# Performance work log

Measured on AMD Instinct MI355X. Metric: run time of the kernel, lower is better.

Reference implementation:

```python
import jax, jax.numpy as jnp
import numpy as np

GROUPS = 32
EPS = 1e-5

def setup_inputs() -> dict:
    key = jax.random.key(0)
    ks = jax.random.split(key, 10)
    B, H, W, C = 2, 64, 64, 512
    s = 1.0 / np.sqrt(C)
    return {
        "x": jax.random.normal(ks[0], (B, H, W, C), dtype=jnp.float32),
        "gamma": jnp.ones((C,), jnp.float32),
        "beta": jnp.zeros((C,), jnp.float32),
        "wq": jax.random.normal(ks[1], (C, C), jnp.float32) * s,
        "bq": jnp.zeros((C,), jnp.float32),
        "wk": jax.random.normal(ks[2], (C, C), jnp.float32) * s,
        "bk": jnp.zeros((C,), jnp.float32),
        "wv": jax.random.normal(ks[3], (C, C), jnp.float32) * s,
        "bv": jnp.zeros((C,), jnp.float32),
        "wp": jax.random.normal(ks[4], (C, C), jnp.float32) * s,
        "bp": jnp.zeros((C,), jnp.float32),
    }

def _group_norm(x, gamma, beta):
    B, H, W, C = x.shape
    xg = x.reshape(B, H, W, GROUPS, C // GROUPS)
    mean = jnp.mean(xg, axis=(1, 2, 4), keepdims=True)
    var = jnp.var(xg, axis=(1, 2, 4), keepdims=True)
    xg = (xg - mean) * jax.lax.rsqrt(var + EPS)
    return xg.reshape(B, H, W, C) * gamma + beta

def reference(x, gamma, beta, wq, bq, wk, bk, wv, bv, wp, bp):
    B, H, W, C = x.shape
    h_ = _group_norm(x, gamma, beta)
    # 1x1 convs are per-pixel linear maps
    q = jnp.einsum("bhwc,cd->bhwd", h_, wq) + bq
    k = jnp.einsum("bhwc,cd->bhwd", h_, wk) + bk
    v = jnp.einsum("bhwc,cd->bhwd", h_, wv) + bv
    q = q.reshape(B, H * W, C)
    k = k.reshape(B, H * W, C)
    v = v.reshape(B, H * W, C)
    scale = C ** (-0.5)
    attn = jax.nn.softmax(jnp.einsum("bqc,bkc->bqk", q, k) * scale, axis=-1)
    out = jnp.einsum("bqk,bkc->bqc", attn, v).reshape(B, H, W, C)
    proj = jnp.einsum("bhwc,cd->bhwd", out, wp) + bp
    return x + proj
```

## Files before the change

### kernel.cpp

```cpp
#include <hip/hip_runtime.h>
#include <hip/hip_bf16.h>
#include <cstdint>
#include <cstddef>

typedef __bf16 bf16;
typedef bf16 bf16x8 __attribute__((ext_vector_type(8)));
typedef bf16 bf16x4 __attribute__((ext_vector_type(4)));
typedef float floatx4 __attribute__((ext_vector_type(4)));
typedef int intx8 __attribute__((ext_vector_type(8)));
typedef int intx4 __attribute__((ext_vector_type(4)));

#define DEVI __device__ __forceinline__

#define C_  512
#define HW_ 4096
#define B_  2
#define M_  8192
#define TK  64


DEVI floatx4 mfma16(bf16x8 a, bf16x8 b, floatx4 c) {
  return __builtin_amdgcn_mfma_f32_16x16x32_bf16(a, b, c, 0, 0, 0);
}

DEVI floatx4 mfma_fp8(intx8 a, intx8 b, floatx4 c) {
  return __builtin_amdgcn_mfma_scale_f32_16x16x128_f8f6f4(a, b, c, 0, 0,
                                                          0, 127, 0, 127);
}

DEVI void gload16(const void* g, void* lds) {
  using gp = const __attribute__((address_space(1))) unsigned int*;
  using lp = __attribute__((address_space(3))) unsigned int*;
  __builtin_amdgcn_global_load_lds(
      reinterpret_cast<gp>(reinterpret_cast<uintptr_t>(g)),
      reinterpret_cast<lp>((unsigned int)(uintptr_t)lds), 16, 0, 0);
}

DEVI uint32_t f32_to_fp8(float x) {
  return (uint32_t)__builtin_amdgcn_cvt_pk_fp8_f32(x, x, 0, false) & 0xffu;
}
DEVI int pack4_fp8(float a, float b, float c, float d) {
  int pk = __builtin_amdgcn_cvt_pk_fp8_f32(a, b, 0, false);
  return __builtin_amdgcn_cvt_pk_fp8_f32(c, d, pk, true);
}

__global__ __launch_bounds__(256) void gn_part(const float* __restrict__ x,
                                               float* __restrict__ pp,
                                               float* __restrict__ l) {
  int blk = blockIdx.x;
  int t = threadIdx.x;
  if (t < 16) l[blk * 16 + t] = 0.f;
  int batch = blk >> 8;
  int pix0 = (blk & 255) * 16;
  int c4 = (t & 127) << 2;
  int ph = t >> 7;
  const float* px = x + (size_t)batch * HW_ * C_ + (size_t)(pix0 + ph) * C_ + c4;
  float s1 = 0.f, s2 = 0.f;
#pragma unroll
  for (int i = 0; i < 8; i++) {
    float4 v = *reinterpret_cast<const float4*>(px + (size_t)i * 2 * C_);
    s1 += v.x + v.y + v.z + v.w;
    s2 += v.x * v.x + v.y * v.y + v.z * v.z + v.w * v.w;
  }
  __shared__ float l1[256], l2[256];
  l1[t] = s1; l2[t] = s2;
  __syncthreads();
  if (t < 32) {
    float a = 0.f, b2 = 0.f;
#pragma unroll
    for (int j = 0; j < 4; j++) {
      a  += l1[t * 4 + j] + l1[t * 4 + j + 128];
      b2 += l2[t * 4 + j] + l2[t * 4 + j + 128];
    }
    pp[blk * 32 + t] = a;
    pp[512 * 32 + blk * 32 + t] = b2;
  }
}

__global__ __launch_bounds__(256) void finish_wtrans(
    const float* __restrict__ pp, float* __restrict__ stats,
    const float* __restrict__ wq, const float* __restrict__ wk,
    const float* __restrict__ wv, const float* __restrict__ wp,
    uint8_t* __restrict__ w8, bf16* __restrict__ wtp) {
  int t = threadIdx.x;
  if (blockIdx.x < 64) {
    int bg = blockIdx.x;
    int b = bg >> 5, g = bg & 31;
    float s1 = pp[(b * 256 + t) * 32 + g];
    float s2 = pp[512 * 32 + (b * 256 + t) * 32 + g];
    for (int off = 32; off; off >>= 1) {
      s1 += __shfl_down(s1, off);
      s2 += __shfl_down(s2, off);
    }
    __shared__ float r1[4], r2[4];
    int wid = t >> 6;
    if ((t & 63) == 0) { r1[wid] = s1; r2[wid] = s2; }
    __syncthreads();
    if (t == 0) {
      s1 = r1[0] + r1[1] + r1[2] + r1[3];
      s2 = r2[0] + r2[1] + r2[2] + r2[3];
      float inv = 1.0f / (HW_ * 16);
      float mean = s1 * inv;
      float var  = s2 * inv - mean * mean;
      stats[bg]      = mean;
      stats[64 + bg] = rsqrtf(var + 1e-5f);
    }
    return;
  }
  int id = blockIdx.x - 64;
  int z = id >> 8;
  int k0 = ((id >> 4) & 15) * 32, n0 = (id & 15) * 32;
  const float* w = (z == 0) ? wq : (z == 1) ? wk : (z == 2) ? wv : wp;
  __shared__ float tt[32][33];
  int r = t >> 5, cc = t & 31;
  for (int i = 0; i < 4; i++) {
    int rr = r + i * 8;
    tt[rr][cc] = w[(size_t)(k0 + rr) * C_ + n0 + cc];
  }
  __syncthreads();
  if (z < 3) {
    uint8_t* dst = w8 + (size_t)z * C_ * C_;
    for (int i = 0; i < 4; i++) {
      int rr = r + i * 8;
      dst[(size_t)(n0 + rr) * C_ + k0 + cc] = (uint8_t)f32_to_fp8(tt[cc][rr]);
    }
  } else {
    for (int i = 0; i < 4; i++) {
      int rr = r + i * 8;
      wtp[(size_t)(n0 + rr) * C_ + k0 + cc] = (bf16)tt[cc][rr];
    }
  }
}

__global__ __launch_bounds__(256) void gn_apply(const float* __restrict__ x,
                                                const float* __restrict__ gamma,
                                                const float* __restrict__ beta,
                                                const float* __restrict__ stats,
                                                uint8_t* __restrict__ h8) {
  int idx = blockIdx.x * 256 + threadIdx.x;
  int m  = idx >> 7;
  int c4 = (idx & 127) << 2;
  int b = m >> 12;
  int g = c4 >> 4;
  float mean = stats[(b << 5) + g];
  float rs   = stats[64 + (b << 5) + g];
  const float4 xv = *reinterpret_cast<const float4*>(x + (size_t)m * C_ + c4);
  const float4 gv = *reinterpret_cast<const float4*>(gamma + c4);
  const float4 bv = *reinterpret_cast<const float4*>(beta + c4);
  int pk = pack4_fp8((xv.x - mean) * rs * gv.x + bv.x,
                     (xv.y - mean) * rs * gv.y + bv.y,
                     (xv.z - mean) * rs * gv.z + bv.z,
                     (xv.w - mean) * rs * gv.w + bv.w);
  *reinterpret_cast<int*>(h8 + (size_t)m * C_ + c4) = pk;
}

template <int BM, int BN, int MT, int NT>
DEVI void gemm_main(const bf16* __restrict__ A, int lda,
                    const bf16* __restrict__ Bt, int ldb,
                    int K, floatx4 (&acc)[MT][NT]) {
  constexpr int WCOLS = BN / (NT * 16);
  __shared__ __align__(16) bf16 As[BM * TK];
  __shared__ __align__(16) bf16 Bs[BN * TK];
  int tid = threadIdx.x;
  int w = tid >> 6, lane = tid & 63;
  int wrow = w / WCOLS, wcol = w % WCOLS;
  int col = lane & 15, quad = lane >> 4;
#pragma unroll
  for (int mt = 0; mt < MT; mt++)
#pragma unroll
    for (int nt = 0; nt < NT; nt++)
      acc[mt][nt] = floatx4{0.f, 0.f, 0.f, 0.f};
  for (int k0 = 0; k0 < K; k0 += TK) {
    __syncthreads();
#pragma unroll
    for (int i = 0; i < BM / 32; i++) {
      int id = tid + i * 256;
      int r = id >> 3, wd = id & 7;
      gload16(A + (size_t)r * lda + k0 + ((wd ^ (r & 7)) << 3), As + id * 8);
    }
#pragma unroll
    for (int i = 0; i < BN / 32; i++) {
      int id = tid + i * 256;
      int r = id >> 3, wd = id & 7;
      gload16(Bt + (size_t)r * ldb + k0 + ((wd ^ (r & 7)) << 3), Bs + id * 8);
    }
    __syncthreads();
#pragma unroll
    for (int kk = 0; kk < 2; kk++) {
      bf16x8 af[MT], bfr[NT];
#pragma unroll
      for (int mt = 0; mt < MT; mt++) {
        int rA = wrow * MT * 16 + mt * 16 + col;
        af[mt] = *reinterpret_cast<const bf16x8*>(
            As + rA * TK + (((kk * 4 + quad) ^ (rA & 7)) << 3));
      }
#pragma unroll
      for (int nt = 0; nt < NT; nt++) {
        int rB = wcol * NT * 16 + nt * 16 + col;
        bfr[nt] = *reinterpret_cast<const bf16x8*>(
            Bs + rB * TK + (((kk * 4 + quad) ^ (rB & 7)) << 3));
      }
#pragma unroll
      for (int mt = 0; mt < MT; mt++)
#pragma unroll
        for (int nt = 0; nt < NT; nt++)
          acc[mt][nt] = mfma16(af[mt], bfr[nt], acc[mt][nt]);
    }
  }
}

template <int BM, int BN, int MT, int NT>
DEVI void gemm_fp8(const uint8_t* __restrict__ A, int lda,
                   const uint8_t* __restrict__ Bt, int ldb,
                   int K, floatx4 (&acc)[MT][NT]) {
  constexpr int WCOLS = BN / (NT * 16);
  __shared__ __align__(16) uint8_t As[BM * 128];
  __shared__ __align__(16) uint8_t Bs[BN * 128];
  int tid = threadIdx.x;
  int w = tid >> 6, lane = tid & 63;
  int wrow = w / WCOLS, wcol = w % WCOLS;
  int col = lane & 15, quad = lane >> 4;
#pragma unroll
  for (int mt = 0; mt < MT; mt++)
#pragma unroll
    for (int nt = 0; nt < NT; nt++)
      acc[mt][nt] = floatx4{0.f, 0.f, 0.f, 0.f};
  for (int k0 = 0; k0 < K; k0 += 128) {
    __syncthreads();
#pragma unroll
    for (int i = 0; i < BM / 32; i++) {
      int id = tid + i * 256;
      int r = id >> 3, wd = id & 7;
      gload16(A + (size_t)r * lda + k0 + ((wd ^ (r & 7)) << 4), As + id * 16);
    }
#pragma unroll
    for (int i = 0; i < BN / 32; i++) {
      int id = tid + i * 256;
      int r = id >> 3, wd = id & 7;
      gload16(Bt + (size_t)r * ldb + k0 + ((wd ^ (r & 7)) << 4), Bs + id * 16);
    }
    __syncthreads();
    intx8 af[MT], bfr[NT];
#pragma unroll
    for (int mt = 0; mt < MT; mt++) {
      int rA = wrow * MT * 16 + mt * 16 + col;
      const uint8_t* rowp = As + (size_t)rA * 128;
      intx4 lo = *reinterpret_cast<const intx4*>(
          rowp + (((2 * quad) ^ (rA & 7)) << 4));
      intx4 hi = *reinterpret_cast<const intx4*>(
          rowp + (((2 * quad + 1) ^ (rA & 7)) << 4));
      af[mt] = __builtin_shufflevector(lo, hi, 0, 1, 2, 3, 4, 5, 6, 7);
    }
#pragma unroll
    for (int nt = 0; nt < NT; nt++) {
      int rB = wcol * NT * 16 + nt * 16 + col;
      const uint8_t* rowp = Bs + (size_t)rB * 128;
      intx4 lo = *reinterpret_cast<const intx4*>(
          rowp + (((2 * quad) ^ (rB & 7)) << 4));
      intx4 hi = *reinterpret_cast<const intx4*>(
          rowp + (((2 * quad + 1) ^ (rB & 7)) << 4));
      bfr[nt] = __builtin_shufflevector(lo, hi, 0, 1, 2, 3, 4, 5, 6, 7);
    }
#pragma unroll
    for (int mt = 0; mt < MT; mt++)
#pragma unroll
      for (int nt = 0; nt < NT; nt++)
        acc[mt][nt] = mfma_fp8(af[mt], bfr[nt], acc[mt][nt]);
  }
}

__global__ __launch_bounds__(256) void gemm_qkv(const uint8_t* __restrict__ h8,
                                                const uint8_t* __restrict__ w8,
                                                const float* __restrict__ bq,
                                                const float* __restrict__ bk,
                                                const float* __restrict__ bv,
                                                uint8_t* __restrict__ q8,
                                                uint8_t* __restrict__ k8,
                                                uint8_t* __restrict__ vt8) {
  int z = blockIdx.z;
  int m0 = blockIdx.x * 128, n0 = blockIdx.y * 128;
  floatx4 acc[4][4];
  gemm_fp8<128, 128, 4, 4>(h8 + (size_t)m0 * C_, C_,
                           w8 + (size_t)z * C_ * C_ + (size_t)n0 * C_, C_, C_, acc);
  int tid = threadIdx.x, w = tid >> 6, lane = tid & 63;
  int wrow = w >> 1, wcol = w & 1;
  int col = lane & 15, quad = lane >> 4;
  const float* bias = (z == 0) ? bq : (z == 1) ? bk : bv;
  if (z < 2) {
    uint8_t* out = (z == 0) ? q8 : k8;
#pragma unroll
    for (int mt = 0; mt < 4; mt++)
#pragma unroll
      for (int nt = 0; nt < 4; nt++) {
        int n = n0 + wcol * 64 + nt * 16 + col;
        float bb = bias[n];
#pragma unroll
        for (int r = 0; r < 4; r++) {
          int m = m0 + wrow * 64 + mt * 16 + quad * 4 + r;
          out[(size_t)m * C_ + n] = (uint8_t)f32_to_fp8(acc[mt][nt][r] + bb);
        }
      }
  } else {
#pragma unroll
    for (int mt = 0; mt < 4; mt++)
#pragma unroll
      for (int nt = 0; nt < 4; nt++) {
        int n = n0 + wcol * 64 + nt * 16 + col;
        float bb = bias[n];
        int mbase = m0 + wrow * 64 + mt * 16 + quad * 4;
        int b = mbase >> 12;
        int s = mbase & 4095;
        int pk = pack4_fp8(acc[mt][nt][0] + bb, acc[mt][nt][1] + bb,
                           acc[mt][nt][2] + bb, acc[mt][nt][3] + bb);
        *reinterpret_cast<int*>(vt8 + ((size_t)b * C_ + n) * HW_ + s) = pk;
      }
  }
}

__global__ __launch_bounds__(256) void gemm_qk(const uint8_t* __restrict__ q8,
                                               const uint8_t* __restrict__ k8,
                                               uint8_t* __restrict__ P8,
                                               float* __restrict__ l) {
  int b = blockIdx.z;
  int fid = blockIdx.y * 32 + blockIdx.x;
  int nid = (fid & 7) * 128 + (fid >> 3);
  int m0 = (nid & 31) * 128, n0 = (nid >> 5) * 128;
  floatx4 acc[4][4];
  gemm_fp8<128, 128, 4, 4>(q8 + ((size_t)b * HW_ + m0) * C_, C_,
                           k8 + ((size_t)b * HW_ + n0) * C_, C_, C_, acc);
  int tid = threadIdx.x, w = tid >> 6, lane = tid & 63;
  int wrow = w >> 1, wcol = w & 1;
  int col = lane & 15, quad = lane >> 4;
  const float sl2e = 0.044194173824159216f * 1.4426950408889634f;
  uint8_t* Pb = P8 + (size_t)b * HW_ * HW_;
  float* lb = l + (size_t)b * HW_;
#pragma unroll
  for (int mt = 0; mt < 4; mt++) {
    float rs[4] = {0.f, 0.f, 0.f, 0.f};
#pragma unroll
    for (int nt = 0; nt < 4; nt++) {
      int n = n0 + wcol * 64 + nt * 16 + col;
      float p0 = exp2f(acc[mt][nt][0] * sl2e);
      float p1 = exp2f(acc[mt][nt][1] * sl2e);
      float p2 = exp2f(acc[mt][nt][2] * sl2e);
      float p3 = exp2f(acc[mt][nt][3] * sl2e);
      int pk = pack4_fp8(p0, p1, p2, p3);
      size_t base = (size_t)(m0 + wrow * 64 + mt * 16 + quad * 4) * HW_ + n;
      Pb[base]           = (uint8_t)pk;
      Pb[base + HW_]     = (uint8_t)((unsigned)pk >> 8);
      Pb[base + 2 * HW_] = (uint8_t)((unsigned)pk >> 16);
      Pb[base + 3 * HW_] = (uint8_t)((unsigned)pk >> 24);
      rs[0] += p0; rs[1] += p1; rs[2] += p2; rs[3] += p3;
    }
#pragma unroll
    for (int off = 1; off < 16; off <<= 1)
#pragma unroll
      for (int r = 0; r < 4; r++)
        rs[r] += __shfl_xor(rs[r], off);
    if (col == 0)
#pragma unroll
      for (int r = 0; r < 4; r++)
        atomicAdd(&lb[m0 + wrow * 64 + mt * 16 + quad * 4 + r], rs[r]);
  }
}

__global__ __launch_bounds__(256) void gemm_pv(const uint8_t* __restrict__ P8,
                                               const uint8_t* __restrict__ vt8,
                                               const float* __restrict__ l,
                                               bf16* __restrict__ o) {
  int b = blockIdx.z;
  int m0 = blockIdx.x * 128, n0 = blockIdx.y * 64;
  floatx4 acc[2][4];
  gemm_fp8<128, 64, 2, 4>(P8 + (size_t)b * HW_ * HW_ + (size_t)m0 * HW_, HW_,
                          vt8 + ((size_t)b * C_ + n0) * HW_, HW_, HW_, acc);
  int tid = threadIdx.x, w = tid >> 6, lane = tid & 63;
  int col = lane & 15, quad = lane >> 4;
  const float* lb = l + (size_t)b * HW_;
  bf16* ob = o + (size_t)b * HW_ * C_;
#pragma unroll
  for (int mt = 0; mt < 2; mt++)
#pragma unroll
    for (int r = 0; r < 4; r++) {
      int m = m0 + w * 32 + mt * 16 + quad * 4 + r;
      float inv = 1.0f / lb[m];
#pragma unroll
      for (int nt = 0; nt < 4; nt++) {
        int n = n0 + nt * 16 + col;
        ob[(size_t)m * C_ + n] = (bf16)(acc[mt][nt][r] * inv);
      }
    }
}

__global__ __launch_bounds__(256) void gemm_proj(const bf16* __restrict__ o,
                                                 const bf16* __restrict__ wtp,
                                                 const float* __restrict__ bp,
                                                 const float* __restrict__ x,
                                                 float* __restrict__ out) {
  int m0 = blockIdx.x * 128, n0 = blockIdx.y * 128;
  floatx4 acc[4][4];
  gemm_main<128, 128, 4, 4>(o + (size_t)m0 * C_, C_, wtp + (size_t)n0 * C_, C_, C_, acc);
  int tid = threadIdx.x, w = tid >> 6, lane = tid & 63;
  int wrow = w >> 1, wcol = w & 1;
  int col = lane & 15, quad = lane >> 4;
#pragma unroll
  for (int mt = 0; mt < 4; mt++)
#pragma unroll
    for (int nt = 0; nt < 4; nt++) {
      int n = n0 + wcol * 64 + nt * 16 + col;
      float bb = bp[n];
#pragma unroll
      for (int r = 0; r < 4; r++) {
        int m = m0 + wrow * 64 + mt * 16 + quad * 4 + r;
        out[(size_t)m * C_ + n] = x[(size_t)m * C_ + n] + acc[mt][nt][r] + bb;
      }
    }
}

extern "C" void kernel_launch(void* const* d_in, const int* in_sizes, int n_in,
                              void* d_out, int out_size, void* d_ws, size_t ws_size,
                              hipStream_t stream) {
  const float* x     = (const float*)d_in[0];
  const float* gamma = (const float*)d_in[1];
  const float* beta  = (const float*)d_in[2];
  const float* wq    = (const float*)d_in[3];
  const float* bq    = (const float*)d_in[4];
  const float* wk    = (const float*)d_in[5];
  const float* bk    = (const float*)d_in[6];
  const float* wv    = (const float*)d_in[7];
  const float* bv    = (const float*)d_in[8];
  const float* wp    = (const float*)d_in[9];
  const float* bp    = (const float*)d_in[10];
  float* out = (float*)d_out;

  char* w8s = (char*)d_ws;
  float* stats = (float*)(w8s);
  float* l     = (float*)(w8s + 65536u);
  float* pp    = (float*)(w8s + 393216u);
  uint8_t* w8  = (uint8_t*)(w8s + (1u << 20));
  bf16* wtp    = (bf16*)(w8s + (2u << 20));
  uint8_t* h8  = (uint8_t*)(w8s + (4u << 20));
  bf16* o      = (bf16*)(w8s + (8u << 20));
  uint8_t* q8  = (uint8_t*)(w8s + (16u << 20));
  uint8_t* k8  = (uint8_t*)(w8s + (20u << 20));
  uint8_t* vt8 = (uint8_t*)(w8s + (24u << 20));
  uint8_t* P8  = (uint8_t*)(w8s + (28u << 20));

  gn_part<<<512, 256, 0, stream>>>(x, pp, l);
  finish_wtrans<<<1088, 256, 0, stream>>>(pp, stats, wq, wk, wv, wp, w8, wtp);
  gn_apply<<<4096, 256, 0, stream>>>(x, gamma, beta, stats, h8);
  gemm_qkv<<<dim3(M_ / 128, C_ / 128, 3), 256, 0, stream>>>(h8, w8, bq, bk, bv, q8, k8, vt8);
  gemm_qk<<<dim3(HW_ / 128, HW_ / 128, B_), 256, 0, stream>>>(q8, k8, P8, l);
  gemm_pv<<<dim3(HW_ / 128, C_ / 64, B_), 256, 0, stream>>>(P8, vt8, l, o);
  gemm_proj<<<dim3(M_ / 128, C_ / 128, 1), 256, 0, stream>>>(o, wtp, bp, x, out);
}
```

Before: 187.2 us.

## Double-buffer LDS in GEMM loops and retile PV GEMM with XCD-aware block mapping

```diff
diff --git a/kernel.cpp b/kernel.cpp
--- a/kernel.cpp
+++ b/kernel.cpp
@@ -159,8 +159,9 @@
                     const bf16* __restrict__ Bt, int ldb,
                     int K, floatx4 (&acc)[MT][NT]) {
   constexpr int WCOLS = BN / (NT * 16);
-  __shared__ __align__(16) bf16 As[BM * TK];
-  __shared__ __align__(16) bf16 Bs[BN * TK];
+  static_assert(BM / 32 + BN / 32 == 8, "vmcnt(8) hardcoded below");
+  __shared__ __align__(16) bf16 As[2][BM * TK];
+  __shared__ __align__(16) bf16 Bs[2][BN * TK];
   int tid = threadIdx.x;
   int w = tid >> 6, lane = tid & 63;
   int wrow = w / WCOLS, wcol = w % WCOLS;
@@ -170,21 +171,22 @@
 #pragma unroll
     for (int nt = 0; nt < NT; nt++)
       acc[mt][nt] = floatx4{0.f, 0.f, 0.f, 0.f};
-  for (int k0 = 0; k0 < K; k0 += TK) {
-    __syncthreads();
+
+  auto stage = [&](int k0, bf16* as, bf16* bs) {
 #pragma unroll
     for (int i = 0; i < BM / 32; i++) {
       int id = tid + i * 256;
       int r = id >> 3, wd = id & 7;
-      gload16(A + (size_t)r * lda + k0 + ((wd ^ (r & 7)) << 3), As + id * 8);
+      gload16(A + (size_t)r * lda + k0 + ((wd ^ (r & 7)) << 3), as + id * 8);
     }
 #pragma unroll
     for (int i = 0; i < BN / 32; i++) {
       int id = tid + i * 256;
       int r = id >> 3, wd = id & 7;
-      gload16(Bt + (size_t)r * ldb + k0 + ((wd ^ (r & 7)) << 3), Bs + id * 8);
-    }
-    __syncthreads();
+      gload16(Bt + (size_t)r * ldb + k0 + ((wd ^ (r & 7)) << 3), bs + id * 8);
+    }
+  };
+  auto compute = [&](const bf16* sa, const bf16* sb) {
 #pragma unroll
     for (int kk = 0; kk < 2; kk++) {
       bf16x8 af[MT], bfr[NT];
@@ -192,13 +194,13 @@
       for (int mt = 0; mt < MT; mt++) {
         int rA = wrow * MT * 16 + mt * 16 + col;
         af[mt] = *reinterpret_cast<const bf16x8*>(
-            As + rA * TK + (((kk * 4 + quad) ^ (rA & 7)) << 3));
+            sa + rA * TK + (((kk * 4 + quad) ^ (rA & 7)) << 3));
       }
 #pragma unroll
       for (int nt = 0; nt < NT; nt++) {
         int rB = wcol * NT * 16 + nt * 16 + col;
         bfr[nt] = *reinterpret_cast<const bf16x8*>(
-            Bs + rB * TK + (((kk * 4 + quad) ^ (rB & 7)) << 3));
+            sb + rB * TK + (((kk * 4 + quad) ^ (rB & 7)) << 3));
       }
 #pragma unroll
       for (int mt = 0; mt < MT; mt++)
@@ -206,7 +208,26 @@
         for (int nt = 0; nt < NT; nt++)
           acc[mt][nt] = mfma16(af[mt], bfr[nt], acc[mt][nt]);
     }
-  }
+  };
+
+  bf16 *s0a = &As[0][0], *s0b = &Bs[0][0];
+  bf16 *s1a = &As[1][0], *s1b = &Bs[1][0];
+  stage(0, s0a, s0b);
+  int nIter = K / TK;
+  for (int t = 0; t < nIter - 1; t++) {
+    stage((t + 1) * TK, s1a, s1b);
+    asm volatile("s_waitcnt vmcnt(8)" ::: "memory");
+    asm volatile("s_barrier" ::: "memory");
+    compute(s0a, s0b);
+    asm volatile("s_waitcnt lgkmcnt(0)" ::: "memory");
+    asm volatile("s_barrier" ::: "memory");
+    bf16* tp;
+    tp = s0a; s0a = s1a; s1a = tp;
+    tp = s0b; s0b = s1b; s1b = tp;
+  }
+  asm volatile("s_waitcnt vmcnt(0)" ::: "memory");
+  asm volatile("s_barrier" ::: "memory");
+  compute(s0a, s0b);
 }
 
 template <int BM, int BN, int MT, int NT>
@@ -214,8 +235,9 @@
                    const uint8_t* __restrict__ Bt, int ldb,
                    int K, floatx4 (&acc)[MT][NT]) {
   constexpr int WCOLS = BN / (NT * 16);
-  __shared__ __align__(16) uint8_t As[BM * 128];
-  __shared__ __align__(16) uint8_t Bs[BN * 128];
+  static_assert(BM / 32 + BN / 32 == 8, "vmcnt(8) hardcoded below");
+  __shared__ __align__(16) uint8_t As[2][BM * 128];
+  __shared__ __align__(16) uint8_t Bs[2][BN * 128];
   int tid = threadIdx.x;
   int w = tid >> 6, lane = tid & 63;
   int wrow = w / WCOLS, wcol = w % WCOLS;
@@ -225,26 +247,27 @@
 #pragma unroll
     for (int nt = 0; nt < NT; nt++)
       acc[mt][nt] = floatx4{0.f, 0.f, 0.f, 0.f};
-  for (int k0 = 0; k0 < K; k0 += 128) {
-    __syncthreads();
+
+  auto stage = [&](int k0, uint8_t* as, uint8_t* bs) {
 #pragma unroll
     for (int i = 0; i < BM / 32; i++) {
       int id = tid + i * 256;
       int r = id >> 3, wd = id & 7;
-      gload16(A + (size_t)r * lda + k0 + ((wd ^ (r & 7)) << 4), As + id * 16);
+      gload16(A + (size_t)r * lda + k0 + ((wd ^ (r & 7)) << 4), as + id * 16);
     }
 #pragma unroll
     for (int i = 0; i < BN / 32; i++) {
       int id = tid + i * 256;
       int r = id >> 3, wd = id & 7;
-      gload16(Bt + (size_t)r * ldb + k0 + ((wd ^ (r & 7)) << 4), Bs + id * 16);
-    }
-    __syncthreads();
+      gload16(Bt + (size_t)r * ldb + k0 + ((wd ^ (r & 7)) << 4), bs + id * 16);
+    }
+  };
+  auto compute = [&](const uint8_t* sa, const uint8_t* sb) {
     intx8 af[MT], bfr[NT];
 #pragma unroll
     for (int mt = 0; mt < MT; mt++) {
       int rA = wrow * MT * 16 + mt * 16 + col;
-      const uint8_t* rowp = As + (size_t)rA * 128;
+      const uint8_t* rowp = sa + (size_t)rA * 128;
       intx4 lo = *reinterpret_cast<const intx4*>(
           rowp + (((2 * quad) ^ (rA & 7)) << 4));
       intx4 hi = *reinterpret_cast<const intx4*>(
@@ -254,7 +277,7 @@
 #pragma unroll
     for (int nt = 0; nt < NT; nt++) {
       int rB = wcol * NT * 16 + nt * 16 + col;
-      const uint8_t* rowp = Bs + (size_t)rB * 128;
+      const uint8_t* rowp = sb + (size_t)rB * 128;
       intx4 lo = *reinterpret_cast<const intx4*>(
           rowp + (((2 * quad) ^ (rB & 7)) << 4));
       intx4 hi = *reinterpret_cast<const intx4*>(
@@ -266,7 +289,26 @@
 #pragma unroll
       for (int nt = 0; nt < NT; nt++)
         acc[mt][nt] = mfma_fp8(af[mt], bfr[nt], acc[mt][nt]);
-  }
+  };
+
+  uint8_t *s0a = &As[0][0], *s0b = &Bs[0][0];
+  uint8_t *s1a = &As[1][0], *s1b = &Bs[1][0];
+  stage(0, s0a, s0b);
+  int nIter = K >> 7;
+  for (int t = 0; t < nIter - 1; t++) {
+    stage((t + 1) << 7, s1a, s1b);
+    asm volatile("s_waitcnt vmcnt(8)" ::: "memory");
+    asm volatile("s_barrier" ::: "memory");
+    compute(s0a, s0b);
+    asm volatile("s_waitcnt lgkmcnt(0)" ::: "memory");
+    asm volatile("s_barrier" ::: "memory");
+    uint8_t* tp;
+    tp = s0a; s0a = s1a; s1a = tp;
+    tp = s0b; s0b = s1b; s1b = tp;
+  }
+  asm volatile("s_waitcnt vmcnt(0)" ::: "memory");
+  asm volatile("s_barrier" ::: "memory");
+  compute(s0a, s0b);
 }
 
 __global__ __launch_bounds__(256) void gemm_qkv(const uint8_t* __restrict__ h8,
@@ -369,23 +411,27 @@
                                                const float* __restrict__ l,
                                                bf16* __restrict__ o) {
   int b = blockIdx.z;
-  int m0 = blockIdx.x * 128, n0 = blockIdx.y * 64;
-  floatx4 acc[2][4];
-  gemm_fp8<128, 64, 2, 4>(P8 + (size_t)b * HW_ * HW_ + (size_t)m0 * HW_, HW_,
-                          vt8 + ((size_t)b * C_ + n0) * HW_, HW_, HW_, acc);
+  int fid = blockIdx.y * 32 + blockIdx.x;
+  int xcd = fid & 7, i = fid >> 3;
+  int m0 = (xcd * 4 + (i & 3)) * 128;
+  int n0 = (i >> 2) * 128;
+  floatx4 acc[4][4];
+  gemm_fp8<128, 128, 4, 4>(P8 + (size_t)b * HW_ * HW_ + (size_t)m0 * HW_, HW_,
+                           vt8 + ((size_t)b * C_ + n0) * HW_, HW_, HW_, acc);
   int tid = threadIdx.x, w = tid >> 6, lane = tid & 63;
+  int wrow = w >> 1, wcol = w & 1;
   int col = lane & 15, quad = lane >> 4;
   const float* lb = l + (size_t)b * HW_;
   bf16* ob = o + (size_t)b * HW_ * C_;
 #pragma unroll
-  for (int mt = 0; mt < 2; mt++)
+  for (int mt = 0; mt < 4; mt++)
 #pragma unroll
     for (int r = 0; r < 4; r++) {
-      int m = m0 + w * 32 + mt * 16 + quad * 4 + r;
+      int m = m0 + wrow * 64 + mt * 16 + quad * 4 + r;
       float inv = 1.0f / lb[m];
 #pragma unroll
       for (int nt = 0; nt < 4; nt++) {
-        int n = n0 + nt * 16 + col;
+        int n = n0 + wcol * 64 + nt * 16 + col;
         ob[(size_t)m * C_ + n] = (bf16)(acc[mt][nt][r] * inv);
       }
     }
@@ -450,6 +496,6 @@
   gn_apply<<<4096, 256, 0, stream>>>(x, gamma, beta, stats, h8);
   gemm_qkv<<<dim3(M_ / 128, C_ / 128, 3), 256, 0, stream>>>(h8, w8, bq, bk, bv, q8, k8, vt8);
   gemm_qk<<<dim3(HW_ / 128, HW_ / 128, B_), 256, 0, stream>>>(q8, k8, P8, l);
-  gemm_pv<<<dim3(HW_ / 128, C_ / 64, B_), 256, 0, stream>>>(P8, vt8, l, o);
+  gemm_pv<<<dim3(HW_ / 128, C_ / 128, B_), 256, 0, stream>>>(P8, vt8, l, o);
   gemm_proj<<<dim3(M_ / 128, C_ / 128, 1), 256, 0, stream>>>(o, wtp, bp, x, out);
 }
```

Result: faster. 177.8 us (-5.0%).
